# Optimization experiments

Hardware: AMD Instinct MI355X
Metric: run time of the kernel (lower is better)

## Reference

```python
import jax, jax.numpy as jnp
import numpy as np

N = 100_000      # nodes
E = 1_600_000    # edges
C_IN = 3         # pos dim
C = 128          # inter_dim == oup_dim
EPS = 1e-5       # BatchNorm eps


def setup_inputs() -> dict:
    key = jax.random.key(0)
    ks = iter(jax.random.split(key, 64))
    inp = {}
    inp['pos'] = jax.random.normal(next(ks), (N, C_IN), dtype=jnp.float32)
    inp['edge_index'] = jax.random.randint(next(ks), (2, E), 0, N, dtype=jnp.int32)
    dims = [C_IN, C, C, C, C]
    for i in range(1, 5):
        cin, cout = dims[i - 1], dims[i]
        inp[f'wl{i}'] = jax.random.normal(next(ks), (cin, cout), jnp.float32) * 0.05
        inp[f'bl{i}'] = jnp.zeros((cout,), jnp.float32)
        inp[f'wr{i}'] = jax.random.normal(next(ks), (cin, cout), jnp.float32) * 0.05
        inp[f'g{i}'] = jax.random.uniform(next(ks), (cout,), jnp.float32, 0.5, 1.5)
        inp[f'be{i}'] = jax.random.normal(next(ks), (cout,), jnp.float32) * 0.1
        inp[f'm{i}'] = jax.random.normal(next(ks), (cout,), jnp.float32) * 0.1
        inp[f'v{i}'] = jax.random.uniform(next(ks), (cout,), jnp.float32, 0.5, 1.5)
    for j, (cin, cout) in enumerate([(C, C), (C, C), (C, C)], start=1):
        inp[f'wf{j}'] = jax.random.normal(next(ks), (cin, cout), jnp.float32) * 0.05
        inp[f'bf{j}'] = jnp.zeros((cout,), jnp.float32)
    return inp


def _sage(x, src, dst, wl, bl, wr):
    # PyG SAGEConv: lin_l(mean_{j->i} x_j) + lin_r(x_i)
    msg_sum = jax.ops.segment_sum(x[src], dst, num_segments=N)          # [N, Cin]
    deg = jax.ops.segment_sum(jnp.ones((src.shape[0], 1), x.dtype), dst, num_segments=N)
    agg = msg_sum / jnp.maximum(deg, 1.0)
    return agg @ wl + bl + x @ wr


def _bn(x, g, b, m, v):
    return g * (x - m) * jax.lax.rsqrt(v + EPS) + b


def reference(pos, edge_index,
              wl1, bl1, wr1, g1, be1, m1, v1,
              wl2, bl2, wr2, g2, be2, m2, v2,
              wl3, bl3, wr3, g3, be3, m3, v3,
              wl4, bl4, wr4, g4, be4, m4, v4,
              wf1, bf1, wf2, bf2, wf3, bf3):
    src, dst = edge_index[0], edge_index[1]
    layers = [(wl1, bl1, wr1, g1, be1, m1, v1),
              (wl2, bl2, wr2, g2, be2, m2, v2),
              (wl3, bl3, wr3, g3, be3, m3, v3),
              (wl4, bl4, wr4, g4, be4, m4, v4)]
    x = pos
    for (wl, bl, wr, g, b, m, v) in layers:
        x = jax.nn.relu(_bn(_sage(x, src, dst, wl, bl, wr), g, b, m, v))
        # dropout p=0.1 inactive at inference
    x = x @ wf1 + bf1
    x = jax.nn.relu(x) @ wf2 + bf2
    x = x @ wf3 + bf3
    return x  # cls=False: raw output, no log_softmax
```

## Files before the change

### kernel.cpp

```cpp
#include <hip/hip_runtime.h>

#define NN 100000
#define EE 1600000
#define CC 128
#define NP 100032
#define NBK 782
#define BCAP 2304

typedef _Float16 f16;
typedef __attribute__((ext_vector_type(2))) f16 f16x2;
typedef __attribute__((ext_vector_type(8))) f16 f16x8;
typedef __attribute__((ext_vector_type(4))) float f32x4;

#define MFMA16(a, b, c) __builtin_amdgcn_mfma_f32_16x16x32_f16(a, b, c, 0, 0, 0)

__global__ __launch_bounds__(1024) void k_part(const int* __restrict__ src,
                                               const int* __restrict__ dst,
                                               int* __restrict__ bcur,
                                               unsigned* __restrict__ bedge) {
  __shared__ int hist[NBK];
  __shared__ int base[NBK];
  const int t = threadIdx.x;
  for (int i = t; i < NBK; i += 1024) hist[i] = 0;
  __syncthreads();
  const int4* src4 = (const int4*)src;
  const int4* dst4 = (const int4*)dst;
  int4 s[4], d[4];
  bool val[4];
#pragma unroll
  for (int w = 0; w < 4; w++) {
    int i4 = blockIdx.x * 4096 + w * 1024 + t;
    val[w] = (i4 < EE / 4);
    if (val[w]) {
      s[w] = src4[i4];
      d[w] = dst4[i4];
      atomicAdd(&hist[d[w].x >> 7], 1);
      atomicAdd(&hist[d[w].y >> 7], 1);
      atomicAdd(&hist[d[w].z >> 7], 1);
      atomicAdd(&hist[d[w].w >> 7], 1);
    }
  }
  __syncthreads();
  for (int i = t; i < NBK; i += 1024) {
    int c = hist[i];
    base[i] = c ? atomicAdd(&bcur[i], c) : 0;
  }
  __syncthreads();
  for (int i = t; i < NBK; i += 1024) hist[i] = 0;
  __syncthreads();
#pragma unroll
  for (int w = 0; w < 4; w++) {
    if (val[w]) {
      int ss[4] = {s[w].x, s[w].y, s[w].z, s[w].w};
      int dd[4] = {d[w].x, d[w].y, d[w].z, d[w].w};
#pragma unroll
      for (int q = 0; q < 4; q++) {
        int b = dd[q] >> 7;
        int p = atomicAdd(&hist[b], 1);
        int slot = base[b] + p;
        if (slot < BCAP)
          bedge[(size_t)b * BCAP + slot] =
              (unsigned)ss[q] | ((unsigned)(dd[q] & 127) << 17);
      }
    }
  }
}

__global__ __launch_bounds__(256) void k_bdeg(const int* __restrict__ bcur,
                                              const unsigned* __restrict__ bedge,
                                              int* __restrict__ degi) {
  __shared__ int h[128];
  const int b = blockIdx.x;
  const int t = threadIdx.x;
  if (t < 128) h[t] = 0;
  __syncthreads();
  const int cnt = min(bcur[b], BCAP);
  const unsigned* be = bedge + (size_t)b * BCAP;
  for (int i = t; i < cnt; i += 256) atomicAdd(&h[(be[i] >> 17) & 127], 1);
  __syncthreads();
  int n = b * 128 + t;
  if (t < 128 && n < NN) degi[n] = h[t];
}

__global__ __launch_bounds__(1024) void k_scan1(const int* __restrict__ degi,
                                                int* __restrict__ bsum) {
  __shared__ int sh[1024];
  int t = threadIdx.x;
  int i = blockIdx.x * 1024 + t;
  sh[t] = (i < NN) ? degi[i] : 0;
  __syncthreads();
  for (int d = 512; d > 0; d >>= 1) {
    if (t < d) sh[t] += sh[t + d];
    __syncthreads();
  }
  if (t == 0) bsum[blockIdx.x] = sh[0];
}

__global__ __launch_bounds__(128) void k_scan2(const int* __restrict__ bsum,
                                               int* __restrict__ bbase,
                                               int* __restrict__ off) {
  __shared__ int sh[128];
  int t = threadIdx.x;
  int v = (t < 98) ? bsum[t] : 0;
  sh[t] = v;
  __syncthreads();
  for (int d = 1; d < 128; d <<= 1) {
    int a = (t >= d) ? sh[t - d] : 0;
    __syncthreads();
    sh[t] += a;
    __syncthreads();
  }
  if (t < 98) bbase[t] = sh[t] - v;
  if (t == 127) off[NN] = sh[127];
}

__global__ __launch_bounds__(1024) void k_scan3(const int* __restrict__ degi,
                                                const int* __restrict__ bbase,
                                                int* __restrict__ off) {
  __shared__ int sh[1024];
  int t = threadIdx.x;
  int i = blockIdx.x * 1024 + t;
  int v = (i < NN) ? degi[i] : 0;
  sh[t] = v;
  __syncthreads();
  for (int d = 1; d < 1024; d <<= 1) {
    int a = (t >= d) ? sh[t - d] : 0;
    __syncthreads();
    sh[t] += a;
    __syncthreads();
  }
  if (i < NN) off[i] = bbase[blockIdx.x] + sh[t] - v;
}

__global__ __launch_bounds__(256) void k_bfill(const int* __restrict__ bcur,
                                               const unsigned* __restrict__ bedge,
                                               const int* __restrict__ off,
                                               int* __restrict__ csr) {
  __shared__ int curs[128];
  __shared__ int offs[128];
  const int b = blockIdx.x;
  const int t = threadIdx.x;
  if (t < 128) {
    int n = b * 128 + t;
    offs[t] = (n < NN) ? off[n] : 0;
    curs[t] = 0;
  }
  __syncthreads();
  const int cnt = min(bcur[b], BCAP);
  const unsigned* be = bedge + (size_t)b * BCAP;
  for (int i = t; i < cnt; i += 256) {
    unsigned u = be[i];
    int node = (u >> 17) & 127;
    int sv = u & 0x1FFFF;
    int p = atomicAdd(&curs[node], 1);
    csr[offs[node] + p] = sv;
  }
}

struct WPtrs { const float* w[9]; };
__global__ __launch_bounds__(256) void k_packw(WPtrs wp, f16* __restrict__ out) {
  int t = blockIdx.x * 256 + threadIdx.x;
  int mat = t >> 14;
  int idx = t & 16383;
  int j = idx & 7;
  int lane = (idx >> 3) & 63;
  int ks = (idx >> 9) & 3;
  int nt = idx >> 11;
  int c16 = lane & 15, quad = lane >> 4;
  int k = ks * 32 + quad * 8 + j;
  int n = nt * 16 + c16;
  out[(size_t)mat * 16384 + idx] = (f16)wp.w[mat][k * CC + n];
}

__global__ __launch_bounds__(256) void k_agg3(const int* __restrict__ off,
                                              const int* __restrict__ csr,
                                              const float* __restrict__ pos,
                                              float* __restrict__ agg3) {
  int n = blockIdx.x * 256 + threadIdx.x;
  if (n >= NN) return;
  int b = off[n], e = off[n + 1];
  float a0 = 0.f, a1 = 0.f, a2 = 0.f;
  for (int i = b; i < e; i++) {
    int s = csr[i];
    a0 += pos[s * 3 + 0];
    a1 += pos[s * 3 + 1];
    a2 += pos[s * 3 + 2];
  }
  float rd = 1.0f / fmaxf((float)(e - b), 1.0f);
  agg3[n * 3 + 0] = a0 * rd;
  agg3[n * 3 + 1] = a1 * rd;
  agg3[n * 3 + 2] = a2 * rd;
}

__global__ __launch_bounds__(128) void k_node1(
    const float* __restrict__ agg3, const float* __restrict__ pos,
    const float* __restrict__ wl, const float* __restrict__ bl,
    const float* __restrict__ wr, const float* __restrict__ g,
    const float* __restrict__ be, const float* __restrict__ bm,
    const float* __restrict__ bv, f16* __restrict__ x) {
  int n = blockIdx.x;
  int c = threadIdx.x;
  __shared__ float sa[3], sp[3];
  if (c < 3) {
    sa[c] = agg3[n * 3 + c];
    sp[c] = pos[n * 3 + c];
  }
  __syncthreads();
  float acc = bl[c];
#pragma unroll
  for (int k = 0; k < 3; k++) {
    acc += sa[k] * wl[k * CC + c];
    acc += sp[k] * wr[k * CC + c];
  }
  float sc = g[c] * rsqrtf(bv[c] + 1e-5f);
  float yv = fmaxf((acc - bm[c]) * sc + be[c], 0.0f);
  x[(size_t)n * CC + c] = (f16)yv;
}

__global__ __launch_bounds__(256) void k_aggregate(const int* __restrict__ off,
                                                   const int* __restrict__ csr,
                                                   const f16* __restrict__ x,
                                                   f16* __restrict__ agg) {
  const int n = blockIdx.x * 4 + (threadIdx.x >> 6);
  const int lane = threadIdx.x & 63;
  const int b = off[n], e = off[n + 1];
  float a0 = 0.f, a1 = 0.f;
  int i = b;
  for (; i + 4 <= e; i += 4) {
    int s0 = csr[i], s1 = csr[i + 1], s2 = csr[i + 2], s3 = csr[i + 3];
    f16x2 v0 = *(const f16x2*)(x + (size_t)s0 * CC + lane * 2);
    f16x2 v1 = *(const f16x2*)(x + (size_t)s1 * CC + lane * 2);
    f16x2 v2 = *(const f16x2*)(x + (size_t)s2 * CC + lane * 2);
    f16x2 v3 = *(const f16x2*)(x + (size_t)s3 * CC + lane * 2);
    a0 += ((float)v0[0] + (float)v1[0]) + ((float)v2[0] + (float)v3[0]);
    a1 += ((float)v0[1] + (float)v1[1]) + ((float)v2[1] + (float)v3[1]);
  }
  for (; i < e; i++) {
    int s = csr[i];
    f16x2 v = *(const f16x2*)(x + (size_t)s * CC + lane * 2);
    a0 += (float)v[0];
    a1 += (float)v[1];
  }
  const float rd = 1.0f / fmaxf((float)(e - b), 1.0f);
  f16x2 o;
  o[0] = (f16)(a0 * rd);
  o[1] = (f16)(a1 * rd);
  *(f16x2*)(agg + (size_t)n * CC + lane * 2) = o;
}

__global__ __launch_bounds__(256) void k_sage_mfma(
    f16* __restrict__ x, const f16* __restrict__ agg,
    const f16* __restrict__ wl, const f16* __restrict__ wr,
    const float* __restrict__ bl, const float* __restrict__ g,
    const float* __restrict__ be, const float* __restrict__ bm,
    const float* __restrict__ bv) {
  const int lane = threadIdx.x & 63;
  const int wave = threadIdx.x >> 6;
  const int c16 = lane & 15;
  const int quad = lane >> 4;
  const int n0 = blockIdx.x * 64 + wave * 16;
  const int rowX = n0 + c16;
  const int rowA = min(rowX, NN - 1);
  const f16* px = x + (size_t)rowX * CC + quad * 8;
  const f16* pa = agg + (size_t)rowA * CC + quad * 8;
  f32x4 acc[8];
#pragma unroll
  for (int t = 0; t < 8; t++) acc[t] = {0.f, 0.f, 0.f, 0.f};
#pragma unroll
  for (int ks = 0; ks < 4; ks++) {
    f16x8 Ax = *(const f16x8*)(px + ks * 32);
    f16x8 Aa = *(const f16x8*)(pa + ks * 32);
#pragma unroll
    for (int nt = 0; nt < 8; nt++) {
      const size_t wo = (size_t)((nt * 4 + ks) * 64 + lane) * 8;
      f16x8 Bl = *(const f16x8*)(wl + wo);
      f16x8 Br = *(const f16x8*)(wr + wo);
      acc[nt] = MFMA16(Aa, Bl, acc[nt]);
      acc[nt] = MFMA16(Ax, Br, acc[nt]);
    }
  }
#pragma unroll
  for (int nt = 0; nt < 8; nt++) {
    const int col = nt * 16 + c16;
    const float blc = bl[col];
    const float sc = g[col] * rsqrtf(bv[col] + 1e-5f);
    const float mm = bm[col];
    const float bb = be[col];
#pragma unroll
    for (int r = 0; r < 4; r++) {
      const int node = n0 + quad * 4 + r;
      if (node < NN) {
        float yv = fmaxf((acc[nt][r] + blc - mm) * sc + bb, 0.0f);
        x[(size_t)node * CC + col] = (f16)yv;
      }
    }
  }
}

__global__ __launch_bounds__(256) void k_dense_fused(
    const f16* __restrict__ x, const f16* __restrict__ w1,
    const f16* __restrict__ w2, const f16* __restrict__ w3,
    const float* __restrict__ b1, const float* __restrict__ b2,
    const float* __restrict__ b3, float* __restrict__ out) {
  const int lane = threadIdx.x & 63;
  const int wave = threadIdx.x >> 6;
  const int c16 = lane & 15;
  const int quad = lane >> 4;
  const int n0 = blockIdx.x * 64 + wave * 16;
  const int lrow = wave * 16;
  __shared__ f16 sh[64][136];

  f32x4 acc[8];
#pragma unroll
  for (int t = 0; t < 8; t++) acc[t] = {0.f, 0.f, 0.f, 0.f};
  const f16* px = x + (size_t)(n0 + c16) * CC + quad * 8;
#pragma unroll
  for (int ks = 0; ks < 4; ks++) {
    f16x8 Ax = *(const f16x8*)(px + ks * 32);
#pragma unroll
    for (int nt = 0; nt < 8; nt++) {
      f16x8 B = *(const f16x8*)(w1 + (size_t)((nt * 4 + ks) * 64 + lane) * 8);
      acc[nt] = MFMA16(Ax, B, acc[nt]);
    }
  }
#pragma unroll
  for (int nt = 0; nt < 8; nt++) {
    const int col = nt * 16 + c16;
    const float bc = b1[col];
#pragma unroll
    for (int r = 0; r < 4; r++)
      sh[lrow + quad * 4 + r][col] = (f16)fmaxf(acc[nt][r] + bc, 0.0f);
  }
  __syncthreads();
#pragma unroll
  for (int t = 0; t < 8; t++) acc[t] = {0.f, 0.f, 0.f, 0.f};
#pragma unroll
  for (int ks = 0; ks < 4; ks++) {
    f16x8 Ax = *(const f16x8*)&sh[lrow + c16][ks * 32 + quad * 8];
#pragma unroll
    for (int nt = 0; nt < 8; nt++) {
      f16x8 B = *(const f16x8*)(w2 + (size_t)((nt * 4 + ks) * 64 + lane) * 8);
      acc[nt] = MFMA16(Ax, B, acc[nt]);
    }
  }
  __syncthreads();
#pragma unroll
  for (int nt = 0; nt < 8; nt++) {
    const int col = nt * 16 + c16;
    const float bc = b2[col];
#pragma unroll
    for (int r = 0; r < 4; r++)
      sh[lrow + quad * 4 + r][col] = (f16)(acc[nt][r] + bc);
  }
  __syncthreads();
#pragma unroll
  for (int t = 0; t < 8; t++) acc[t] = {0.f, 0.f, 0.f, 0.f};
#pragma unroll
  for (int ks = 0; ks < 4; ks++) {
    f16x8 Ax = *(const f16x8*)&sh[lrow + c16][ks * 32 + quad * 8];
#pragma unroll
    for (int nt = 0; nt < 8; nt++) {
      f16x8 B = *(const f16x8*)(w3 + (size_t)((nt * 4 + ks) * 64 + lane) * 8);
      acc[nt] = MFMA16(Ax, B, acc[nt]);
    }
  }
#pragma unroll
  for (int nt = 0; nt < 8; nt++) {
    const int col = nt * 16 + c16;
    const float bc = b3[col];
#pragma unroll
    for (int r = 0; r < 4; r++) {
      const int node = n0 + quad * 4 + r;
      if (node < NN) out[(size_t)node * CC + col] = acc[nt][r] + bc;
    }
  }
}

extern "C" void kernel_launch(void* const* d_in, const int* in_sizes, int n_in,
                              void* d_out, int out_size, void* d_ws,
                              size_t ws_size, hipStream_t stream) {
  const float* pos = (const float*)d_in[0];
  const int* ei = (const int*)d_in[1];
  const int* src = ei;
  const int* dst = ei + EE;
  auto P = [&](int i) { return (const float*)d_in[i]; };

  int* bcur = (int*)d_ws;
  int* off = bcur + NBK;
  int* degi = off + NN + 2;
  int* bsum = degi + NN;
  int* bbase = bsum + 128;
  unsigned* bedge = (unsigned*)(bbase + 128);
  int* csr = (int*)(bedge + (size_t)NBK * BCAP);
  f16* wp16 = (f16*)(csr + EE);
  f16* x = wp16 + 9 * 16384;

  f16* agg = (f16*)d_out;

  hipMemsetAsync(bcur, 0, NBK * sizeof(int), stream);

  k_part<<<(EE / 4 + 4095) / 4096, 1024, 0, stream>>>(src, dst, bcur, bedge);
  k_bdeg<<<NBK, 256, 0, stream>>>(bcur, bedge, degi);
  const int SB = (NN + 1023) / 1024;
  k_scan1<<<SB, 1024, 0, stream>>>(degi, bsum);
  k_scan2<<<1, 128, 0, stream>>>(bsum, bbase, off);
  k_scan3<<<SB, 1024, 0, stream>>>(degi, bbase, off);
  k_bfill<<<NBK, 256, 0, stream>>>(bcur, bedge, off, csr);

  WPtrs wp;
  const int wsrc[9] = {9, 11, 16, 18, 23, 25, 30, 32, 34};
  for (int i = 0; i < 9; i++) wp.w[i] = P(wsrc[i]);
  k_packw<<<(9 * 16384) / 256, 256, 0, stream>>>(wp, wp16);

  k_agg3<<<(NN + 255) / 256, 256, 0, stream>>>(off, csr, pos, (float*)d_out);
  k_node1<<<NN, 128, 0, stream>>>((const float*)d_out, pos, P(2), P(3), P(4),
                                  P(5), P(6), P(7), P(8), x);

  const int NB = NP / 64;
  for (int l = 1; l < 4; l++) {
    int base = 2 + 7 * l;
    int mat = (l - 1) * 2;
    k_aggregate<<<NN / 4, 256, 0, stream>>>(off, csr, x, agg);
    k_sage_mfma<<<NB, 256, 0, stream>>>(
        x, agg, wp16 + (size_t)mat * 16384, wp16 + (size_t)(mat + 1) * 16384,
        P(base + 1), P(base + 3), P(base + 4), P(base + 5), P(base + 6));
  }

  k_dense_fused<<<NB, 256, 0, stream>>>(x, wp16 + (size_t)6 * 16384,
                                        wp16 + (size_t)7 * 16384,
                                        wp16 + (size_t)8 * 16384, P(31), P(33),
                                        P(35), (float*)d_out);
}
```

Before: 603.3 us.

## Fuse neighbor aggregation into SAGE MFMA kernels and fold last layer into dense tail

Each SAGE layer now gathers neighbor means into shared memory inside the MFMA kernel, so the separate aggregate kernel and its global agg buffer round trip go away. Ping-pong x buffers replace in-place updates, since other blocks still read the input rows during the gather. The last SAGE layer is fused with the three dense layers into one tail kernel, and the block-wide barriers are dropped because each wave only touches its own 16 rows. The trade-off is less gather parallelism per block (one wave walks 16 nodes in sequence) and higher shared-memory and register pressure, which may cost occupancy.

```diff
diff --git a/kernel.cpp b/kernel.cpp
--- a/kernel.cpp
+++ b/kernel.cpp
@@ -217,59 +217,67 @@
   x[(size_t)n * CC + c] = (f16)yv;
 }
 
-__global__ __launch_bounds__(256) void k_aggregate(const int* __restrict__ off,
-                                                   const int* __restrict__ csr,
-                                                   const f16* __restrict__ x,
-                                                   f16* __restrict__ agg) {
-  const int n = blockIdx.x * 4 + (threadIdx.x >> 6);
-  const int lane = threadIdx.x & 63;
-  const int b = off[n], e = off[n + 1];
+__device__ __forceinline__ void gather_node(const int* __restrict__ off,
+                                            const int* __restrict__ csr,
+                                            const f16* __restrict__ x, int node,
+                                            int lane, f16* __restrict__ ldsrow) {
   float a0 = 0.f, a1 = 0.f;
-  int i = b;
-  for (; i + 4 <= e; i += 4) {
-    int s0 = csr[i], s1 = csr[i + 1], s2 = csr[i + 2], s3 = csr[i + 3];
-    f16x2 v0 = *(const f16x2*)(x + (size_t)s0 * CC + lane * 2);
-    f16x2 v1 = *(const f16x2*)(x + (size_t)s1 * CC + lane * 2);
-    f16x2 v2 = *(const f16x2*)(x + (size_t)s2 * CC + lane * 2);
-    f16x2 v3 = *(const f16x2*)(x + (size_t)s3 * CC + lane * 2);
-    a0 += ((float)v0[0] + (float)v1[0]) + ((float)v2[0] + (float)v3[0]);
-    a1 += ((float)v0[1] + (float)v1[1]) + ((float)v2[1] + (float)v3[1]);
-  }
-  for (; i < e; i++) {
-    int s = csr[i];
-    f16x2 v = *(const f16x2*)(x + (size_t)s * CC + lane * 2);
-    a0 += (float)v[0];
-    a1 += (float)v[1];
-  }
-  const float rd = 1.0f / fmaxf((float)(e - b), 1.0f);
+  if (node < NN) {
+    const int b = off[node], e = off[node + 1];
+    int i = b;
+    for (; i + 4 <= e; i += 4) {
+      int s0 = csr[i], s1 = csr[i + 1], s2 = csr[i + 2], s3 = csr[i + 3];
+      f16x2 v0 = *(const f16x2*)(x + (size_t)s0 * CC + lane * 2);
+      f16x2 v1 = *(const f16x2*)(x + (size_t)s1 * CC + lane * 2);
+      f16x2 v2 = *(const f16x2*)(x + (size_t)s2 * CC + lane * 2);
+      f16x2 v3 = *(const f16x2*)(x + (size_t)s3 * CC + lane * 2);
+      a0 += ((float)v0[0] + (float)v1[0]) + ((float)v2[0] + (float)v3[0]);
+      a1 += ((float)v0[1] + (float)v1[1]) + ((float)v2[1] + (float)v3[1]);
+    }
+    for (; i < e; i++) {
+      int s = csr[i];
+      f16x2 v = *(const f16x2*)(x + (size_t)s * CC + lane * 2);
+      a0 += (float)v[0];
+      a1 += (float)v[1];
+    }
+    const float rd = 1.0f / fmaxf((float)(e - b), 1.0f);
+    a0 *= rd;
+    a1 *= rd;
+  }
   f16x2 o;
-  o[0] = (f16)(a0 * rd);
-  o[1] = (f16)(a1 * rd);
-  *(f16x2*)(agg + (size_t)n * CC + lane * 2) = o;
-}
-
-__global__ __launch_bounds__(256) void k_sage_mfma(
-    f16* __restrict__ x, const f16* __restrict__ agg,
+  o[0] = (f16)a0;
+  o[1] = (f16)a1;
+  *(f16x2*)(ldsrow + lane * 2) = o;
+}
+
+__global__ __launch_bounds__(256) void k_sage_fused(
+    const int* __restrict__ off, const int* __restrict__ csr,
+    const f16* __restrict__ xin, f16* __restrict__ xout,
     const f16* __restrict__ wl, const f16* __restrict__ wr,
     const float* __restrict__ bl, const float* __restrict__ g,
     const float* __restrict__ be, const float* __restrict__ bm,
     const float* __restrict__ bv) {
   const int lane = threadIdx.x & 63;
   const int wave = threadIdx.x >> 6;
+  const int n0 = blockIdx.x * 64;
+  __shared__ f16 sag[64][136];
+
+#pragma unroll 1
+  for (int i = 0; i < 16; i++) {
+    int lrow = wave * 16 + i;
+    gather_node(off, csr, xin, n0 + lrow, lane, &sag[lrow][0]);
+  }
   const int c16 = lane & 15;
   const int quad = lane >> 4;
-  const int n0 = blockIdx.x * 64 + wave * 16;
-  const int rowX = n0 + c16;
-  const int rowA = min(rowX, NN - 1);
-  const f16* px = x + (size_t)rowX * CC + quad * 8;
-  const f16* pa = agg + (size_t)rowA * CC + quad * 8;
+  const int lbase = wave * 16;
+  const f16* px = xin + (size_t)(n0 + lbase + c16) * CC + quad * 8;
   f32x4 acc[8];
 #pragma unroll
   for (int t = 0; t < 8; t++) acc[t] = {0.f, 0.f, 0.f, 0.f};
 #pragma unroll
   for (int ks = 0; ks < 4; ks++) {
     f16x8 Ax = *(const f16x8*)(px + ks * 32);
-    f16x8 Aa = *(const f16x8*)(pa + ks * 32);
+    f16x8 Aa = *(const f16x8*)&sag[lbase + c16][ks * 32 + quad * 8];
 #pragma unroll
     for (int nt = 0; nt < 8; nt++) {
       const size_t wo = (size_t)((nt * 4 + ks) * 64 + lane) * 8;
@@ -288,35 +296,73 @@
     const float bb = be[col];
 #pragma unroll
     for (int r = 0; r < 4; r++) {
-      const int node = n0 + quad * 4 + r;
+      const int node = n0 + lbase + quad * 4 + r;
       if (node < NN) {
         float yv = fmaxf((acc[nt][r] + blc - mm) * sc + bb, 0.0f);
-        x[(size_t)node * CC + col] = (f16)yv;
+        xout[(size_t)node * CC + col] = (f16)yv;
       }
     }
   }
 }
 
-__global__ __launch_bounds__(256) void k_dense_fused(
-    const f16* __restrict__ x, const f16* __restrict__ w1,
-    const f16* __restrict__ w2, const f16* __restrict__ w3,
-    const float* __restrict__ b1, const float* __restrict__ b2,
-    const float* __restrict__ b3, float* __restrict__ out) {
+__global__ __launch_bounds__(256) void k_tail(
+    const int* __restrict__ off, const int* __restrict__ csr,
+    const f16* __restrict__ xin, const f16* __restrict__ wl,
+    const f16* __restrict__ wr, const float* __restrict__ bl,
+    const float* __restrict__ g, const float* __restrict__ be,
+    const float* __restrict__ bm, const float* __restrict__ bv,
+    const f16* __restrict__ w1, const f16* __restrict__ w2,
+    const f16* __restrict__ w3, const float* __restrict__ b1,
+    const float* __restrict__ b2, const float* __restrict__ b3,
+    float* __restrict__ out) {
   const int lane = threadIdx.x & 63;
   const int wave = threadIdx.x >> 6;
+  const int n0 = blockIdx.x * 64;
+  __shared__ f16 sag[64][136];
+
+#pragma unroll 1
+  for (int i = 0; i < 16; i++) {
+    int lrow = wave * 16 + i;
+    gather_node(off, csr, xin, n0 + lrow, lane, &sag[lrow][0]);
+  }
   const int c16 = lane & 15;
   const int quad = lane >> 4;
-  const int n0 = blockIdx.x * 64 + wave * 16;
-  const int lrow = wave * 16;
-  __shared__ f16 sh[64][136];
-
+  const int lbase = wave * 16;
+  const f16* px = xin + (size_t)(n0 + lbase + c16) * CC + quad * 8;
   f32x4 acc[8];
 #pragma unroll
   for (int t = 0; t < 8; t++) acc[t] = {0.f, 0.f, 0.f, 0.f};
-  const f16* px = x + (size_t)(n0 + c16) * CC + quad * 8;
 #pragma unroll
   for (int ks = 0; ks < 4; ks++) {
     f16x8 Ax = *(const f16x8*)(px + ks * 32);
+    f16x8 Aa = *(const f16x8*)&sag[lbase + c16][ks * 32 + quad * 8];
+#pragma unroll
+    for (int nt = 0; nt < 8; nt++) {
+      const size_t wo = (size_t)((nt * 4 + ks) * 64 + lane) * 8;
+      f16x8 Bl = *(const f16x8*)(wl + wo);
+      f16x8 Br = *(const f16x8*)(wr + wo);
+      acc[nt] = MFMA16(Aa, Bl, acc[nt]);
+      acc[nt] = MFMA16(Ax, Br, acc[nt]);
+    }
+  }
+#pragma unroll
+  for (int nt = 0; nt < 8; nt++) {
+    const int col = nt * 16 + c16;
+    const float blc = bl[col];
+    const float sc = g[col] * rsqrtf(bv[col] + 1e-5f);
+    const float mm = bm[col];
+    const float bb = be[col];
+#pragma unroll
+    for (int r = 0; r < 4; r++) {
+      float yv = fmaxf((acc[nt][r] + blc - mm) * sc + bb, 0.0f);
+      sag[lbase + quad * 4 + r][col] = (f16)yv;
+    }
+  }
+#pragma unroll
+  for (int t = 0; t < 8; t++) acc[t] = {0.f, 0.f, 0.f, 0.f};
+#pragma unroll
+  for (int ks = 0; ks < 4; ks++) {
+    f16x8 Ax = *(const f16x8*)&sag[lbase + c16][ks * 32 + quad * 8];
 #pragma unroll
     for (int nt = 0; nt < 8; nt++) {
       f16x8 B = *(const f16x8*)(w1 + (size_t)((nt * 4 + ks) * 64 + lane) * 8);
@@ -329,35 +375,32 @@
     const float bc = b1[col];
 #pragma unroll
     for (int r = 0; r < 4; r++)
-      sh[lrow + quad * 4 + r][col] = (f16)fmaxf(acc[nt][r] + bc, 0.0f);
-  }
-  __syncthreads();
+      sag[lbase + quad * 4 + r][col] = (f16)fmaxf(acc[nt][r] + bc, 0.0f);
+  }
 #pragma unroll
   for (int t = 0; t < 8; t++) acc[t] = {0.f, 0.f, 0.f, 0.f};
 #pragma unroll
   for (int ks = 0; ks < 4; ks++) {
-    f16x8 Ax = *(const f16x8*)&sh[lrow + c16][ks * 32 + quad * 8];
+    f16x8 Ax = *(const f16x8*)&sag[lbase + c16][ks * 32 + quad * 8];
 #pragma unroll
     for (int nt = 0; nt < 8; nt++) {
       f16x8 B = *(const f16x8*)(w2 + (size_t)((nt * 4 + ks) * 64 + lane) * 8);
       acc[nt] = MFMA16(Ax, B, acc[nt]);
     }
   }
-  __syncthreads();
 #pragma unroll
   for (int nt = 0; nt < 8; nt++) {
     const int col = nt * 16 + c16;
     const float bc = b2[col];
 #pragma unroll
     for (int r = 0; r < 4; r++)
-      sh[lrow + quad * 4 + r][col] = (f16)(acc[nt][r] + bc);
-  }
-  __syncthreads();
+      sag[lbase + quad * 4 + r][col] = (f16)(acc[nt][r] + bc);
+  }
 #pragma unroll
   for (int t = 0; t < 8; t++) acc[t] = {0.f, 0.f, 0.f, 0.f};
 #pragma unroll
   for (int ks = 0; ks < 4; ks++) {
-    f16x8 Ax = *(const f16x8*)&sh[lrow + c16][ks * 32 + quad * 8];
+    f16x8 Ax = *(const f16x8*)&sag[lbase + c16][ks * 32 + quad * 8];
 #pragma unroll
     for (int nt = 0; nt < 8; nt++) {
       f16x8 B = *(const f16x8*)(w3 + (size_t)((nt * 4 + ks) * 64 + lane) * 8);
@@ -370,7 +413,7 @@
     const float bc = b3[col];
 #pragma unroll
     for (int r = 0; r < 4; r++) {
-      const int node = n0 + quad * 4 + r;
+      const int node = n0 + lbase + quad * 4 + r;
       if (node < NN) out[(size_t)node * CC + col] = acc[nt][r] + bc;
     }
   }
@@ -393,9 +436,8 @@
   unsigned* bedge = (unsigned*)(bbase + 128);
   int* csr = (int*)(bedge + (size_t)NBK * BCAP);
   f16* wp16 = (f16*)(csr + EE);
-  f16* x = wp16 + 9 * 16384;
-
-  f16* agg = (f16*)d_out;
+  f16* xa = wp16 + 9 * 16384;
+  f16* xb = xa + (size_t)NP * CC;
 
   hipMemsetAsync(bcur, 0, NBK * sizeof(int), stream);
 
@@ -414,20 +456,19 @@
 
   k_agg3<<<(NN + 255) / 256, 256, 0, stream>>>(off, csr, pos, (float*)d_out);
   k_node1<<<NN, 128, 0, stream>>>((const float*)d_out, pos, P(2), P(3), P(4),
-                                  P(5), P(6), P(7), P(8), x);
+                                  P(5), P(6), P(7), P(8), xa);
 
   const int NB = NP / 64;
-  for (int l = 1; l < 4; l++) {
-    int base = 2 + 7 * l;
-    int mat = (l - 1) * 2;
-    k_aggregate<<<NN / 4, 256, 0, stream>>>(off, csr, x, agg);
-    k_sage_mfma<<<NB, 256, 0, stream>>>(
-        x, agg, wp16 + (size_t)mat * 16384, wp16 + (size_t)(mat + 1) * 16384,
-        P(base + 1), P(base + 3), P(base + 4), P(base + 5), P(base + 6));
-  }
-
-  k_dense_fused<<<NB, 256, 0, stream>>>(x, wp16 + (size_t)6 * 16384,
-                                        wp16 + (size_t)7 * 16384,
-                                        wp16 + (size_t)8 * 16384, P(31), P(33),
-                                        P(35), (float*)d_out);
-}
+  k_sage_fused<<<NB, 256, 0, stream>>>(off, csr, xa, xb, wp16 + (size_t)0 * 16384,
+                                       wp16 + (size_t)1 * 16384, P(10), P(12),
+                                       P(13), P(14), P(15));
+  k_sage_fused<<<NB, 256, 0, stream>>>(off, csr, xb, xa, wp16 + (size_t)2 * 16384,
+                                       wp16 + (size_t)3 * 16384, P(17), P(19),
+                                       P(20), P(21), P(22));
+  k_tail<<<NB, 256, 0, stream>>>(off, csr, xa, wp16 + (size_t)4 * 16384,
+                                 wp16 + (size_t)5 * 16384, P(24), P(26), P(27),
+                                 P(28), P(29), wp16 + (size_t)6 * 16384,
+                                 wp16 + (size_t)7 * 16384,
+                                 wp16 + (size_t)8 * 16384, P(31), P(33), P(35),
+                                 (float*)d_out);
+}
```

Result: slower. 744.8 us (+23.5%).
